# Performance work log

Hardware: AMD Instinct MI355X
Metric: run time of the kernel (lower is better)

The kernel has to match this reference:

```python
import jax, jax.numpy as jnp
import numpy as np

K_WAVE = 15.0  # wavenumber k from source
EPS_R = 1e-8   # epsilon in dr/dn denominator from source


def bessel_j1(x):
    # Numerical-Recipes rational/asymptotic approximation of J1(x).
    ax = jnp.abs(x)
    y = x * x
    num = x * (72362614232.0 + y * (-7895059235.0 + y * (242396853.1 + y * (-2972611.439 + y * (15704.48260 + y * (-30.16036606))))))
    den = 144725228442.0 + y * (2300535178.0 + y * (18583304.74 + y * (99447.43394 + y * (376.9991397 + y))))
    small = num / den
    axs = jnp.maximum(ax, 1e-20)
    z = 8.0 / axs
    y2 = z * z
    xx = axs - 2.356194491
    p1 = 1.0 + y2 * (0.183105e-2 + y2 * (-0.3516396496e-4 + y2 * (0.2457520174e-5 + y2 * (-0.240337019e-6))))
    p2 = 0.04687499995 + y2 * (-0.2002690873e-3 + y2 * (0.8449199096e-5 + y2 * (-0.88228987e-6 + y2 * 0.105787412e-6)))
    large = jnp.sqrt(0.636619772 / axs) * (jnp.cos(xx) * p1 - z * jnp.sin(xx) * p2) * jnp.sign(x)
    return jnp.where(ax < 8.0, small, large)


def bessel_y1(x):
    # Numerical-Recipes approximation of Y1(x), x > 0.
    xs = jnp.maximum(x, 1e-12)
    y = xs * xs
    num = xs * (-4.900604943e13 + y * (1.275274390e13 + y * (-5.153438139e11 + y * (7.349264551e9 + y * (-4.237922726e7 + y * 8.511937935e4)))))
    den = 2.499580570e14 + y * (4.244419664e12 + y * (3.733650367e10 + y * (2.245904002e8 + y * (1.020426050e6 + y * (3.549632885e3 + y)))))
    small = num / den + 0.636619772 * (bessel_j1(xs) * jnp.log(xs) - 1.0 / xs)
    z = 8.0 / xs
    y2 = z * z
    xx = xs - 2.356194491
    p1 = 1.0 + y2 * (0.183105e-2 + y2 * (-0.3516396496e-4 + y2 * (0.2457520174e-5 + y2 * (-0.240337019e-6))))
    p2 = 0.04687499995 + y2 * (-0.2002690873e-3 + y2 * (0.8449199096e-5 + y2 * (-0.88228987e-6 + y2 * 0.105787412e-6)))
    large = jnp.sqrt(0.636619772 / xs) * (jnp.sin(xx) * p1 + z * jnp.cos(xx) * p2)
    return jnp.where(xs < 8.0, small, large)


def _mlp(pts, W1, b1, W2, b2, W3, b3, W4, b4, W5, b5):
    h = jnp.tanh(pts @ W1 + b1)
    h = jnp.tanh(h @ W2 + b2)
    h = jnp.tanh(h @ W3 + b3)
    h = jnp.tanh(h @ W4 + b4)
    return (h @ W5 + b5)[:, 0]  # [M]


def setup_inputs() -> dict:
    key = jax.random.key(0)
    ks = jax.random.split(key, 12)
    N = 1024            # points per side (source uses 50)
    P = 16384           # query points
    H = 50              # hidden width (source default)
    cords = np.linspace(0.0001, 0.9999, N, dtype=np.float32)
    z = np.zeros(N, dtype=np.float32)
    o = np.ones(N, dtype=np.float32)
    top = np.stack([cords, o], 1)
    bottom = np.stack([cords, z], 1)
    left = np.stack([z, cords], 1)
    right = np.stack([o, cords], 1)
    boundary_points = jnp.asarray(np.concatenate([top, bottom, left, right], 0))  # [4N,2]
    nrm = np.concatenate([
        np.stack([z, o], 1),    # top normal (0,1)
        np.stack([z, -o], 1),   # bottom (0,-1)
        np.stack([-o, z], 1),   # left (-1,0)
        np.stack([o, z], 1),    # right (1,0)
    ], 0)
    normals = jnp.asarray(nrm)
    dy = jnp.float32(1.0 / (N - 1))
    points = jax.random.uniform(ks[0], (P, 2), dtype=jnp.float32)
    def lin(k, fin, fout):
        lim = np.sqrt(6.0 / (fin + fout)).astype(np.float32)
        return jax.random.uniform(k, (fin, fout), minval=-lim, maxval=lim, dtype=jnp.float32)
    return {
        'points': points,
        'boundary_points': boundary_points,
        'normals': normals,
        'dy': dy,
        'W1': lin(ks[1], 2, H), 'b1': jnp.zeros((H,), jnp.float32),
        'W2': lin(ks[2], H, H), 'b2': jnp.zeros((H,), jnp.float32),
        'W3': lin(ks[3], H, H), 'b3': jnp.zeros((H,), jnp.float32),
        'W4': lin(ks[4], H, H), 'b4': jnp.zeros((H,), jnp.float32),
        'W5': lin(ks[5], H, 1), 'b5': jnp.zeros((1,), jnp.float32),
    }


def reference(points, boundary_points, normals, dy, W1, b1, W2, b2, W3, b3, W4, b4, W5, b5):
    # density values on the boundary from the MLP
    h_vals = _mlp(boundary_points, W1, b1, W2, b2, W3, b3, W4, b4, W5, b5)  # [M]
    # pairwise geometry: [P, M, 2]
    diff = points[:, None, :] - boundary_points[None, :, :]
    r = jnp.sqrt(jnp.sum(diff * diff, axis=-1))               # [P, M]
    dr_dn = jnp.sum(diff * normals[None, :, :], axis=-1) / (r + EPS_R)
    # Re[-(i/4)*k*H1^{(1)}(k r)] = (k/4)*Y1(k r); output is the real part only,
    # so the J1 (imaginary) component never contributes to the returned value.
    y1 = jax.lax.stop_gradient(bessel_y1(K_WAVE * r))  # hankel term is detached in torch (numpy round-trip)
    green_real = 0.25 * K_WAVE * y1 * dr_dn                   # [P, M]
    u_real = jnp.sum(green_real * h_vals[None, :], axis=-1) * dy  # [P]
    return u_real
```

## Files before the change

kernel.cpp:

```cpp
#include <hip/hip_runtime.h>
#include <math.h>

#define H 50
#define TPB 256
#define MCHUNK 128
#define N_TAB 1368
#define K_WAVE 15.0f

__device__ double j1_d(double x) {
    double ax = fabs(x);
    double y = x * x;
    double num = x * (72362614232.0 + y * (-7895059235.0 + y * (242396853.1 + y * (-2972611.439 + y * (15704.48260 + y * (-30.16036606))))));
    double den = 144725228442.0 + y * (2300535178.0 + y * (18583304.74 + y * (99447.43394 + y * (376.9991397 + y))));
    double small = num / den;
    double axs = fmax(ax, 1e-20);
    double z = 8.0 / axs;
    double y2 = z * z;
    double xx = axs - 2.356194491;
    double p1 = 1.0 + y2 * (0.183105e-2 + y2 * (-0.3516396496e-4 + y2 * (0.2457520174e-5 + y2 * (-0.240337019e-6))));
    double p2 = 0.04687499995 + y2 * (-0.2002690873e-3 + y2 * (0.8449199096e-5 + y2 * (-0.88228987e-6 + y2 * 0.105787412e-6)));
    double large = sqrt(0.636619772 / axs) * (cos(xx) * p1 - z * sin(xx) * p2) * (x < 0.0 ? -1.0 : 1.0);
    return (ax < 8.0) ? small : large;
}

__device__ double y1_d(double x) {
    double xs = fmax(x, 1e-12);
    double y = xs * xs;
    double num = xs * (-4.900604943e13 + y * (1.275274390e13 + y * (-5.153438139e11 + y * (7.349264551e9 + y * (-4.237922726e7 + y * 8.511937935e4)))));
    double den = 2.499580570e14 + y * (4.244419664e12 + y * (3.733650367e10 + y * (2.245904002e8 + y * (1.020426050e6 + y * (3.549632885e3 + y)))));
    double small = num / den + 0.636619772 * (j1_d(xs) * log(xs) - 1.0 / xs);
    double z = 8.0 / xs;
    double y2 = z * z;
    double xx = xs - 2.356194491;
    double p1 = 1.0 + y2 * (0.183105e-2 + y2 * (-0.3516396496e-4 + y2 * (0.2457520174e-5 + y2 * (-0.240337019e-6))));
    double p2 = 0.04687499995 + y2 * (-0.2002690873e-3 + y2 * (0.8449199096e-5 + y2 * (-0.88228987e-6 + y2 * 0.105787412e-6)));
    double large = sqrt(0.636619772 / xs) * (sin(xx) * p1 + z * cos(xx) * p2);
    return (xs < 8.0) ? small : large;
}

__global__ void init_table(float2* __restrict__ tab) {
    int i = blockIdx.x * blockDim.x + threadIdx.x;
    if (i >= N_TAB) return;
    const double dxt = 1.0 / 64.0;
    double x0 = i * dxt, x1 = (i + 1) * dxt;
    double g0 = (i == 0) ? -0.6366197723675814 : x0 * y1_d(x0);
    double g1 = x1 * y1_d(x1);
    tab[i] = make_float2((float)g0, (float)(g1 - g0));
}

__global__ __launch_bounds__(256) void mlp_kernel(
    const float* __restrict__ bp,
    const float* __restrict__ W1, const float* __restrict__ b1,
    const float* __restrict__ W2, const float* __restrict__ b2,
    const float* __restrict__ W3, const float* __restrict__ b3,
    const float* __restrict__ W4, const float* __restrict__ b4,
    const float* __restrict__ W5, const float* __restrict__ b5,
    const float* __restrict__ dyp,
    float* __restrict__ h_out, int M)
{
    __shared__ float ha[4][56];
    __shared__ float hb[4][56];
    int wave = threadIdx.x >> 6;
    int j = threadIdx.x & 63;
    int m = blockIdx.x * 4 + wave;
    if (m >= M) return;
    float px = bp[2 * m], py = bp[2 * m + 1];

    if (j < H) {
        ha[wave][j] = tanhf(fmaf(px, W1[j], fmaf(py, W1[H + j], b1[j])));
    }
    __syncthreads();
    if (j < H) {
        float s = b2[j];
        #pragma unroll
        for (int i = 0; i < H; ++i) s = fmaf(ha[wave][i], W2[i * H + j], s);
        hb[wave][j] = tanhf(s);
    }
    __syncthreads();
    if (j < H) {
        float s = b3[j];
        #pragma unroll
        for (int i = 0; i < H; ++i) s = fmaf(hb[wave][i], W3[i * H + j], s);
        ha[wave][j] = tanhf(s);
    }
    __syncthreads();
    if (j < H) {
        float s = b4[j];
        #pragma unroll
        for (int i = 0; i < H; ++i) s = fmaf(ha[wave][i], W4[i * H + j], s);
        hb[wave][j] = tanhf(s);
    }
    __syncthreads();
    if (j == 0) {
        float s = b5[0];
        #pragma unroll
        for (int i = 0; i < H; ++i) s = fmaf(hb[wave][i], W5[i], s);
        h_out[m] = s * (0.25f * dyp[0]);
    }
}

__global__ __launch_bounds__(TPB, 8) void pair_kernel(
    const float* __restrict__ pts,
    const float* __restrict__ hs,
    const float2* __restrict__ tab,
    float* __restrict__ out, int P)
{
    __shared__ float2 lt[N_TAB];
    for (int i = threadIdx.x; i < N_TAB; i += TPB) lt[i] = tab[i];
    __syncthreads();

    int p = blockIdx.x * TPB + threadIdx.x;
    if (p >= P) return;
    float px = pts[2 * p], py = pts[2 * p + 1];

    int chunk = blockIdx.y;
    int side = chunk >> 3;
    int j0 = (chunk & 7) * MCHUNK;

    float v, w, sgn;
    if (side == 0)      { v = px; w = py - 1.0f; sgn =  1.0f; }
    else if (side == 1) { v = px; w = py;        sgn = -1.0f; }
    else if (side == 2) { v = py; w = px;        sgn = -1.0f; }
    else                { v = py; w = px - 1.0f; sgn =  1.0f; }
    float w2 = w * w;

    const float step = 0.9998f / 1023.0f;
    float dx = v - fmaf((float)j0, step, 0.0001f);
    const float* hp = hs + side * 1024 + j0;

    const float SCL = 64.0f * K_WAVE;
    float acc = 0.0f;
    #pragma unroll 4
    for (int j = 0; j < MCHUNK; ++j) {
        float r2 = fmaxf(fmaf(dx, dx, w2), 1e-12f);
        float ir = __builtin_amdgcn_rsqf(r2);
        float t = r2 * ir * SCL;
        int   i = (int)t;
        float f = __builtin_amdgcn_fractf(t);
        float2 gs = lt[i];
        float g = fmaf(f, gs.y, gs.x);
        acc = fmaf(g * hp[j], ir * ir, acc);
        dx -= step;
    }
    atomicAdd(&out[p], acc * w * sgn);
}

extern "C" void kernel_launch(void* const* d_in, const int* in_sizes, int n_in,
                              void* d_out, int out_size, void* d_ws, size_t ws_size,
                              hipStream_t stream) {
    const float* pts = (const float*)d_in[0];
    const float* bp  = (const float*)d_in[1];
    const float* dyp = (const float*)d_in[3];
    const float* W1 = (const float*)d_in[4];  const float* b1 = (const float*)d_in[5];
    const float* W2 = (const float*)d_in[6];  const float* b2 = (const float*)d_in[7];
    const float* W3 = (const float*)d_in[8];  const float* b3 = (const float*)d_in[9];
    const float* W4 = (const float*)d_in[10]; const float* b4 = (const float*)d_in[11];
    const float* W5 = (const float*)d_in[12]; const float* b5 = (const float*)d_in[13];

    int P = in_sizes[0] / 2;
    int M = in_sizes[1] / 2;

    float*  hs  = (float*)d_ws;
    float2* tab = (float2*)((char*)d_ws + (size_t)M * 4);

    hipMemsetAsync(d_out, 0, (size_t)out_size * sizeof(float), stream);

    init_table<<<(N_TAB + 255) / 256, 256, 0, stream>>>(tab);

    mlp_kernel<<<dim3((M + 3) / 4), dim3(256), 0, stream>>>(
        bp, W1, b1, W2, b2, W3, b3, W4, b4, W5, b5, dyp, hs, M);

    dim3 grid((P + TPB - 1) / TPB, (M / MCHUNK));
    pair_kernel<<<grid, dim3(TPB), 0, stream>>>(pts, hs, tab, (float*)d_out, P);
}
```

Before: 115.3 us.

## Assign one wavefront per query point and reduce with shuffles instead of atomics

The pair kernel now maps each 64-lane wavefront to a single query point. Lanes stride across all four boundary sides, and the partial sums are combined with an xor-shuffle reduction that writes the output directly, so the memset and atomicAdd go away. The lookup table is split into two float arrays to avoid float2 LDS loads. In exchange, the grid becomes 4096 blocks that each reload the 11 KB table into shared memory (previously 64x32 blocks), lanes within a wave now hit scattered table entries, and per-point geometry work is repeated across lanes.

```diff
diff --git a/kernel.cpp b/kernel.cpp
--- a/kernel.cpp
+++ b/kernel.cpp
@@ -3,9 +3,10 @@
 
 #define H 50
 #define TPB 256
-#define MCHUNK 128
 #define N_TAB 1368
 #define K_WAVE 15.0f
+#define NSIDE 1024
+#define STEP (0.9998f / 1023.0f)
 
 __device__ double j1_d(double x) {
     double ax = fabs(x);
@@ -38,14 +39,15 @@
     return (xs < 8.0) ? small : large;
 }
 
-__global__ void init_table(float2* __restrict__ tab) {
+__global__ void init_table(float* __restrict__ tab) {
     int i = blockIdx.x * blockDim.x + threadIdx.x;
     if (i >= N_TAB) return;
     const double dxt = 1.0 / 64.0;
     double x0 = i * dxt, x1 = (i + 1) * dxt;
     double g0 = (i == 0) ? -0.6366197723675814 : x0 * y1_d(x0);
     double g1 = x1 * y1_d(x1);
-    tab[i] = make_float2((float)g0, (float)(g1 - g0));
+    tab[i] = (float)g0;
+    tab[N_TAB + i] = (float)(g1 - g0);
 }
 
 __global__ __launch_bounds__(256) void mlp_kernel(
@@ -102,47 +104,52 @@
 __global__ __launch_bounds__(TPB, 8) void pair_kernel(
     const float* __restrict__ pts,
     const float* __restrict__ hs,
-    const float2* __restrict__ tab,
+    const float* __restrict__ tab,
     float* __restrict__ out, int P)
 {
-    __shared__ float2 lt[N_TAB];
-    for (int i = threadIdx.x; i < N_TAB; i += TPB) lt[i] = tab[i];
+    __shared__ float lt[2 * N_TAB];
+    for (int i = threadIdx.x; i < 2 * N_TAB; i += TPB) lt[i] = tab[i];
     __syncthreads();
 
-    int p = blockIdx.x * TPB + threadIdx.x;
+    int wave = threadIdx.x >> 6;
+    int lane = threadIdx.x & 63;
+    int p = blockIdx.x * 4 + wave;
     if (p >= P) return;
+
     float px = pts[2 * p], py = pts[2 * p + 1];
 
-    int chunk = blockIdx.y;
-    int side = chunk >> 3;
-    int j0 = (chunk & 7) * MCHUNK;
+    const float SCL = 64.0f * K_WAVE;
+    float total = 0.0f;
 
-    float v, w, sgn;
-    if (side == 0)      { v = px; w = py - 1.0f; sgn =  1.0f; }
-    else if (side == 1) { v = px; w = py;        sgn = -1.0f; }
-    else if (side == 2) { v = py; w = px;        sgn = -1.0f; }
-    else                { v = py; w = px - 1.0f; sgn =  1.0f; }
-    float w2 = w * w;
+    #pragma unroll
+    for (int side = 0; side < 4; ++side) {
+        float v, w, sgn;
+        if (side == 0)      { v = px; w = py - 1.0f; sgn =  1.0f; }
+        else if (side == 1) { v = px; w = py;        sgn = -1.0f; }
+        else if (side == 2) { v = py; w = px;        sgn = -1.0f; }
+        else                { v = py; w = px - 1.0f; sgn =  1.0f; }
+        float w2 = w * w;
+        float dx = v - 0.0001f - (float)lane * STEP;
+        const float* hp = hs + side * NSIDE + lane;
+        float acc = 0.0f;
+        #pragma unroll 4
+        for (int t = 0; t < NSIDE / 64; ++t) {
+            float r2 = fmaxf(fmaf(dx, dx, w2), 1e-12f);
+            float ir = __builtin_amdgcn_rsqf(r2);
+            float tt = r2 * ir * SCL;
+            int   i = (int)tt;
+            float f = __builtin_amdgcn_fractf(tt);
+            float g = fmaf(f, lt[i + N_TAB], lt[i]);
+            acc = fmaf(g * hp[t * 64], ir * ir, acc);
+            dx -= 64.0f * STEP;
+        }
+        total = fmaf(acc, w * sgn, total);
+    }
 
-    const float step = 0.9998f / 1023.0f;
-    float dx = v - fmaf((float)j0, step, 0.0001f);
-    const float* hp = hs + side * 1024 + j0;
-
-    const float SCL = 64.0f * K_WAVE;
-    float acc = 0.0f;
-    #pragma unroll 4
-    for (int j = 0; j < MCHUNK; ++j) {
-        float r2 = fmaxf(fmaf(dx, dx, w2), 1e-12f);
-        float ir = __builtin_amdgcn_rsqf(r2);
-        float t = r2 * ir * SCL;
-        int   i = (int)t;
-        float f = __builtin_amdgcn_fractf(t);
-        float2 gs = lt[i];
-        float g = fmaf(f, gs.y, gs.x);
-        acc = fmaf(g * hp[j], ir * ir, acc);
-        dx -= step;
-    }
-    atomicAdd(&out[p], acc * w * sgn);
+    #pragma unroll
+    for (int off = 32; off >= 1; off >>= 1)
+        total += __shfl_xor(total, off, 64);
+    if (lane == 0) out[p] = total;
 }
 
 extern "C" void kernel_launch(void* const* d_in, const int* in_sizes, int n_in,
@@ -160,16 +167,14 @@
     int P = in_sizes[0] / 2;
     int M = in_sizes[1] / 2;
 
-    float*  hs  = (float*)d_ws;
-    float2* tab = (float2*)((char*)d_ws + (size_t)M * 4);
-
-    hipMemsetAsync(d_out, 0, (size_t)out_size * sizeof(float), stream);
+    float* hs  = (float*)d_ws;
+    float* tab = (float*)((char*)d_ws + (size_t)M * 4);
 
     init_table<<<(N_TAB + 255) / 256, 256, 0, stream>>>(tab);
 
     mlp_kernel<<<dim3((M + 3) / 4), dim3(256), 0, stream>>>(
         bp, W1, b1, W2, b2, W3, b3, W4, b4, W5, b5, dyp, hs, M);
 
-    dim3 grid((P + TPB - 1) / TPB, (M / MCHUNK));
-    pair_kernel<<<grid, dim3(TPB), 0, stream>>>(pts, hs, tab, (float*)d_out, P);
+    pair_kernel<<<dim3((P + 3) / 4), dim3(TPB), 0, stream>>>(
+        pts, hs, tab, (float*)d_out, P);
 }
```

Result: no change. 116.3 us (+0.8%).
